# Kernel optimization log

Measured on AMD Instinct MI355X. Metric: run time of the kernel, lower is better.

Reference implementation:

```python
import jax, jax.numpy as jnp
import numpy as np

B, S, W = 16, 256, 128            # batch, seq_len (word pieces), words per sentence
V, H, L, NH, DH, FF, C = 30522, 768, 12, 12, 64, 3072, 425
EPS = 1e-12                        # HF Bert LayerNorm eps


def setup_inputs() -> dict:
    key = jax.random.key(0)
    kiter = iter(jax.random.split(key, 64))
    nk = lambda: next(kiter)
    # each word maps to 1 or 2 word-pieces -> total pieces in [W, 2W] <= S
    word_piece_tracked = jax.random.randint(nk(), (B, W), 1, 3)
    lengths = jnp.sum(word_piece_tracked, axis=1)
    encoded_batch = jax.random.randint(nk(), (B, S), 0, V)
    mask = (jnp.arange(S)[None, :] < lengths[:, None]).astype(jnp.int32)
    p = lambda *shape: jax.random.normal(nk(), shape, jnp.float32) * 0.02
    return dict(
        encoded_batch=encoded_batch, mask=mask, word_piece_tracked=word_piece_tracked,
        word_emb=p(V, H), pos_emb=p(S, H), type_emb=p(1, H),
        emb_ln_s=jnp.ones((H,), jnp.float32), emb_ln_b=jnp.zeros((H,), jnp.float32),
        Wq=p(L, H, H), bq=p(L, H), Wk=p(L, H, H), bk=p(L, H),
        Wv=p(L, H, H), bv=p(L, H), Wo=p(L, H, H), bo=p(L, H),
        ln1_s=jnp.ones((L, H), jnp.float32), ln1_b=jnp.zeros((L, H), jnp.float32),
        Wi=p(L, H, FF), bi=p(L, FF), Wo2=p(L, FF, H), bo2=p(L, H),
        ln2_s=jnp.ones((L, H), jnp.float32), ln2_b=jnp.zeros((L, H), jnp.float32),
        w1=p(H, 1024), b1=p(1024), w2=p(1024, C), b2=p(C),
    )


def _layer_norm(x, s, b):
    mu = jnp.mean(x, -1, keepdims=True)
    var = jnp.var(x, -1, keepdims=True)
    return (x - mu) * jax.lax.rsqrt(var + EPS) * s + b


def _forward(encoded_batch, mask, word_piece_tracked,
             word_emb, pos_emb, type_emb, emb_ln_s, emb_ln_b,
             Wq, bq, Wk, bk, Wv, bv, Wo, bo, ln1_s, ln1_b,
             Wi, bi, Wo2, bo2, ln2_s, ln2_b, w1, b1, w2, b2):
    # BERT embeddings (token_type all zeros)
    x = word_emb[encoded_batch] + pos_emb[None, :, :] + type_emb[0]
    x = _layer_norm(x, emb_ln_s, emb_ln_b)
    attn_bias = (1.0 - mask.astype(jnp.float32))[:, None, None, :] * -10000.0
    scale = 1.0 / np.sqrt(DH).astype(np.float32)

    def step(h, lp):
        wq, bq_, wk, bk_, wv, bv_, wo, bo_, l1s, l1b, wi, bi_, wo2, bo2_, l2s, l2b = lp
        q = (h @ wq + bq_).reshape(B, S, NH, DH)
        k = (h @ wk + bk_).reshape(B, S, NH, DH)
        v = (h @ wv + bv_).reshape(B, S, NH, DH)
        att = jax.nn.softmax(jnp.einsum('bqhd,bkhd->bhqk', q, k) * scale + attn_bias, axis=-1)
        ctx = jnp.einsum('bhqk,bkhd->bqhd', att, v).reshape(B, S, H)
        h = _layer_norm(h + ctx @ wo + bo_, l1s, l1b)
        ff = jax.nn.gelu(h @ wi + bi_, approximate=False)
        h = _layer_norm(h + ff @ wo2 + bo2_, l2s, l2b)
        return h, None

    x, _ = jax.lax.scan(step, x, (Wq, bq, Wk, bk, Wv, bv, Wo, bo, ln1_s, ln1_b,
                                  Wi, bi, Wo2, bo2, ln2_s, ln2_b))

    # MLP head (dropout = identity in eval)
    f1 = jax.nn.relu(x) @ w1 + b1          # [B, S, 1024]
    f2 = jax.nn.relu(f1) @ w2 + b2          # [B, S, C]

    # ragged segment-mean pooling over word pieces (equiv. to the python loop)
    cum = jnp.cumsum(word_piece_tracked, axis=1)                         # [B, W]
    seg = jax.vmap(lambda c: jnp.searchsorted(c, jnp.arange(S), side='right'))(cum)  # [B, S]
    sums = jax.vmap(lambda f, s: jax.ops.segment_sum(f, s, num_segments=W))(f2, seg)
    pooled = sums / word_piece_tracked[..., None].astype(f2.dtype)       # [B, W, C]
    out = jnp.concatenate([pooled, f2[:, W:, :]], axis=1)                # [B, S, C]
    return jax.nn.softmax(out, axis=2)


def reference(encoded_batch, mask, word_piece_tracked,
              word_emb, pos_emb, type_emb, emb_ln_s, emb_ln_b,
              Wq, bq, Wk, bk, Wv, bv, Wo, bo, ln1_s, ln1_b,
              Wi, bi, Wo2, bo2, ln2_s, ln2_b, w1, b1, w2, b2):
    return _forward(encoded_batch, mask, word_piece_tracked,
                    word_emb, pos_emb, type_emb, emb_ln_s, emb_ln_b,
                    Wq, bq, Wk, bk, Wv, bv, Wo, bo, ln1_s, ln1_b,
                    Wi, bi, Wo2, bo2, ln2_s, ln2_b, w1, b1, w2, b2)
```

## Files before the change

### kernel.cpp

```cpp
#include <hip/hip_runtime.h>
#include <math.h>

#define BB 16
#define SS 256
#define WW 128
#define HH 768
#define LL 12
#define NHH 12
#define DHH 64
#define FFD 3072
#define CC 425
#define NTOK (BB*SS)
#define QKVN (3*HH)

typedef __attribute__((ext_vector_type(8))) short bf16x8;
typedef __attribute__((ext_vector_type(4))) float f32x4;

__device__ __forceinline__ float bf2f(unsigned short u) {
    union { unsigned int i; float f; } z; z.i = ((unsigned int)u) << 16; return z.f;
}
__device__ __forceinline__ unsigned short f2bf(float f) {
    union { float f; unsigned int i; } z; z.f = f;
    unsigned int i = z.i;
    unsigned int r = (i + 0x7fffu + ((i >> 16) & 1u)) >> 16;
    return (unsigned short)r;
}

__device__ __forceinline__ void gload16(const void* g, void* l) {
    __builtin_amdgcn_global_load_lds((const __attribute__((address_space(1))) void*)g,
                                     (__attribute__((address_space(3))) void*)l, 16, 0, 0);
}

__device__ __forceinline__ float gelu_f(float v) {
    float ax = fabsf(v) * 0.70710678118654752f;
    float t = 1.0f / fmaf(0.3275911f, ax, 1.0f);
    float poly = t * fmaf(t, fmaf(t, fmaf(t, fmaf(t, 1.061405429f, -1.453152027f),
                                          1.421413741f), -0.284496736f), 0.254829592f);
    float er = 1.0f - poly * __expf(-ax * ax);
    er = (v < 0.f) ? -er : er;
    return 0.5f * v * (1.0f + er);
}

template<int BM, int BN, int ACT_C>
__launch_bounds__(256)
__global__ void gemm_bt(const unsigned short* __restrict__ A,
                        const unsigned short* __restrict__ Bt,
                        const float* __restrict__ bias,
                        unsigned short* __restrict__ Cm,
                        int M, int N, int K, int ldC) {
    constexpr bool BIG = (BM == 128 && BN == 128);
    constexpr int FM = BIG ? 4 : BM / 32;
    constexpr int FN = BIG ? 4 : BN / 32;
    constexpr int ASZ = BM * 32, BSZ = BN * 32;
    __shared__ __align__(16) unsigned short lA[2 * ASZ];
    __shared__ __align__(16) unsigned short lB[2 * BSZ];
    const int tid = threadIdx.x, w = tid >> 6, l = tid & 63;

    const int gx = gridDim.x;
    const int nwg = gx * gridDim.y;
    const int orig = blockIdx.y * gx + blockIdx.x;
    const int q = nwg >> 3, r = nwg & 7, xc = orig & 7, o8 = orig >> 3;
    const int wg = (xc < r ? xc * (q + 1) : r * (q + 1) + (xc - r) * q) + o8;
    const int m0 = (wg / gx) * BM, n0 = (wg % gx) * BN;

    const int wr = BIG ? (w >> 1) * 64 : (w >> 1) * (BM / 2);
    const int wc = BIG ? (w & 1) * 64 : (w & 1) * (BN / 2);
    const int lr = l & 15, lk = (l >> 4) * 8;
    const int rsw = ((lr >> 1) & 3) << 4;
    const int lrow = l >> 2;
    const int gs = (l & 3) ^ ((lrow >> 1) & 3);

    f32x4 acc[FM][FN];
#pragma unroll
    for (int m = 0; m < FM; ++m)
#pragma unroll
        for (int n = 0; n < FN; ++n) acc[m][n] = (f32x4){0.f, 0.f, 0.f, 0.f};

    auto stage = [&](int k0, unsigned short* dA, unsigned short* dB) {
#pragma unroll
        for (int it = 0; it < BM / 64; ++it) {
            int c = w * (BM / 64) + it;
            gload16(A + (size_t)(m0 + c * 16 + lrow) * K + k0 + gs * 8, dA + c * 512);
        }
#pragma unroll
        for (int it = 0; it < BN / 64; ++it) {
            int c = w * (BN / 64) + it;
            gload16(Bt + (size_t)(n0 + c * 16 + lrow) * K + k0 + gs * 8, dB + c * 512);
        }
    };

    const int nt = K >> 5;
    stage(0, lA, lB);
    __syncthreads();

    for (int t = 0; t < nt; ++t) {
        unsigned short* cA = lA + (t & 1) * ASZ;
        unsigned short* cB = lB + (t & 1) * BSZ;
        if (t + 1 < nt)
            stage((t + 1) << 5, lA + ((t + 1) & 1) * ASZ, lB + ((t + 1) & 1) * BSZ);
        bf16x8 af[FM], bfr[FN];
#pragma unroll
        for (int m = 0; m < FM; ++m) {
            int row = wr + m * 16 + lr;
            af[m] = *(const bf16x8*)((const char*)cA + row * 64 + ((lk * 2) ^ rsw));
        }
#pragma unroll
        for (int n = 0; n < FN; ++n) {
            int row = wc + n * 16 + lr;
            bfr[n] = *(const bf16x8*)((const char*)cB + row * 64 + ((lk * 2) ^ rsw));
        }
#pragma unroll
        for (int m = 0; m < FM; ++m)
#pragma unroll
            for (int n = 0; n < FN; ++n)
                acc[m][n] = __builtin_amdgcn_mfma_f32_16x16x32_bf16(af[m], bfr[n], acc[m][n], 0, 0, 0);
        __syncthreads();
    }

    const int orow = (l >> 4) * 4, ocol = l & 15;
#pragma unroll
    for (int m = 0; m < FM; ++m)
#pragma unroll
        for (int n = 0; n < FN; ++n) {
            int c = n0 + wc + n * 16 + ocol;
            if (c >= N) continue;
            float bb = bias[c];
#pragma unroll
            for (int j = 0; j < 4; ++j) {
                int rr = m0 + wr + m * 16 + orow + j;
                float vv = acc[m][n][j] + bb;
                if (ACT_C == 1) vv = gelu_f(vv);
                if (ACT_C == 2) vv = fmaxf(vv, 0.f);
                Cm[(size_t)rr * ldC + c] = f2bf(vv);
            }
        }
}

template<int ACT_A, int ACT_C>
__launch_bounds__(256)
__global__ void gemm_aw(const unsigned short* __restrict__ A,
                        const float* __restrict__ Wm,
                        const float* __restrict__ bias,
                        unsigned short* __restrict__ Cm,
                        int M, int N, int K, int ldC) {
    __shared__ __align__(16) unsigned short lA[64][40];
    __shared__ __align__(16) unsigned short lB[64][40];
    const int tid = threadIdx.x;
    const int m0 = blockIdx.y * 64;
    const int n0 = blockIdx.x * 64;
    const int w = tid >> 6, l = tid & 63;
    const int wr = (w >> 1) * 32, wc = (w & 1) * 32;
    const int lr = l & 15, lk = (l >> 4) * 8;

    f32x4 acc[2][2];
#pragma unroll
    for (int m = 0; m < 2; ++m)
#pragma unroll
        for (int n = 0; n < 2; ++n) acc[m][n] = (f32x4){0.f, 0.f, 0.f, 0.f};

    const int arow = tid >> 2, akc = (tid & 3) << 3;
    const int bkr = tid >> 3, bnc = (tid & 7) << 3;
    const bool nvec = (N & 7) == 0;

    for (int k0 = 0; k0 < K; k0 += 32) {
        uint4 av = *(const uint4*)(A + (size_t)(m0 + arow) * K + (k0 + akc));
        if (ACT_A) {
            unsigned short* p = (unsigned short*)&av;
#pragma unroll
            for (int j = 0; j < 8; ++j) if (p[j] & 0x8000u) p[j] = 0;
        }
        *(uint4*)&lA[arow][akc] = av;
        unsigned short bv[8];
        if (nvec) {
            const float* wp = Wm + (size_t)(k0 + bkr) * N + (n0 + bnc);
            float4 w0 = *(const float4*)(wp);
            float4 w1 = *(const float4*)(wp + 4);
            bv[0] = f2bf(w0.x); bv[1] = f2bf(w0.y); bv[2] = f2bf(w0.z); bv[3] = f2bf(w0.w);
            bv[4] = f2bf(w1.x); bv[5] = f2bf(w1.y); bv[6] = f2bf(w1.z); bv[7] = f2bf(w1.w);
        } else {
#pragma unroll
            for (int j = 0; j < 8; ++j) {
                int col = n0 + bnc + j;
                bv[j] = (col < N) ? f2bf(Wm[(size_t)(k0 + bkr) * N + col]) : (unsigned short)0;
            }
        }
#pragma unroll
        for (int j = 0; j < 8; ++j) lB[bnc + j][bkr] = bv[j];
        __syncthreads();

        bf16x8 af[2], bfr[2];
#pragma unroll
        for (int m = 0; m < 2; ++m) af[m] = *(const bf16x8*)&lA[wr + m * 16 + lr][lk];
#pragma unroll
        for (int n = 0; n < 2; ++n) bfr[n] = *(const bf16x8*)&lB[wc + n * 16 + lr][lk];
#pragma unroll
        for (int m = 0; m < 2; ++m)
#pragma unroll
            for (int n = 0; n < 2; ++n)
                acc[m][n] = __builtin_amdgcn_mfma_f32_16x16x32_bf16(af[m], bfr[n], acc[m][n], 0, 0, 0);
        __syncthreads();
    }

    const int orow = (l >> 4) * 4, ocol = l & 15;
#pragma unroll
    for (int m = 0; m < 2; ++m)
#pragma unroll
        for (int n = 0; n < 2; ++n) {
            int c = n0 + wc + n * 16 + ocol;
            if (c >= N) continue;
            float bb = bias[c];
#pragma unroll
            for (int j = 0; j < 4; ++j) {
                int r = m0 + wr + m * 16 + orow + j;
                float vv = acc[m][n][j] + bb;
                if (ACT_C == 1) vv = gelu_f(vv);
                if (ACT_C == 2) vv = fmaxf(vv, 0.f);
                Cm[(size_t)r * ldC + c] = f2bf(vv);
            }
        }
}

__global__ void transpose_w(const float* __restrict__ src, unsigned short* __restrict__ dst,
                            int K, int N, long srcLS, long dstLS) {
    int n0 = blockIdx.x * 32, k0 = blockIdx.y * 32;
    src += (size_t)blockIdx.z * srcLS;
    dst += (size_t)blockIdx.z * dstLS;
    __shared__ float tile[32][33];
    int tx = threadIdx.x & 31, ty = threadIdx.x >> 5;
#pragma unroll
    for (int r = 0; r < 4; ++r) {
        int k = k0 + ty + r * 8, n = n0 + tx;
        tile[ty + r * 8][tx] = (n < N && k < K) ? src[(size_t)k * N + n] : 0.f;
    }
    __syncthreads();
    int col2 = threadIdx.x & 15, rowb = threadIdx.x >> 4;
#pragma unroll
    for (int p = 0; p < 2; ++p) {
        int n = n0 + rowb + p * 16;
        unsigned int lo = f2bf(tile[col2 * 2][rowb + p * 16]);
        unsigned int hi = f2bf(tile[col2 * 2 + 1][rowb + p * 16]);
        *(unsigned int*)(dst + (size_t)n * K + k0 + col2 * 2) = lo | (hi << 16);
    }
}

__global__ void concat_bias(const float* bq, const float* bk, const float* bv, float* bqkv) {
    int i = blockIdx.x * 256 + threadIdx.x;
    if (i >= LL * QKVN) return;
    int lyr = i / QKVN, c = i % QKVN;
    float v = (c < HH) ? bq[lyr * HH + c] : (c < 2 * HH) ? bk[lyr * HH + c - HH] : bv[lyr * HH + c - 2 * HH];
    bqkv[i] = v;
}

__global__ void build_maskbias(const int* mask, float* mb) {
    int i = blockIdx.x * 256 + threadIdx.x;
    mb[i] = mask[i] ? 0.0f : -10000.0f;
}

__launch_bounds__(256)
__global__ void attention_mfma(const unsigned short* __restrict__ qkv,
                               const float* __restrict__ mb,
                               unsigned short* __restrict__ ctx) {
    const int qt = blockIdx.x, h = blockIdx.y, b = blockIdx.z;
    const int tid = threadIdx.x, w = tid >> 6, l = tid & 63;
    __shared__ __align__(16) unsigned short lK[SS * DHH];
    __shared__ __align__(16) unsigned short lVt[DHH * SS];
    const size_t tokbase = (size_t)b * SS * QKVN;

    {
        const unsigned short* kp = qkv + tokbase + (size_t)tid * QKVN + HH + h * DHH;
        const unsigned short* vp = kp + HH;
#pragma unroll
        for (int c = 0; c < 8; ++c) {
            uint4 kd = *(const uint4*)(kp + c * 8);
            *(uint4*)((char*)lK + ((tid * 128 + c * 16) ^ ((tid & 7) << 4))) = kd;
            uint4 vd = *(const uint4*)(vp + c * 8);
            const unsigned short* e = (const unsigned short*)&vd;
#pragma unroll
            for (int j = 0; j < 8; ++j) {
                int d = c * 8 + j;
                *(unsigned short*)((char*)lVt + ((d * 512 + tid * 2) ^ ((d & 7) << 4))) = e[j];
            }
        }
    }
    const int q0w = qt * 64 + w * 16;
    const unsigned short* qp = qkv + tokbase + (size_t)(q0w + (l & 15)) * QKVN + h * DHH + (l >> 4) * 8;
    bf16x8 aq0 = *(const bf16x8*)(qp);
    bf16x8 aq1 = *(const bf16x8*)(qp + 32);
    __syncthreads();

    f32x4 sc[16];
#pragma unroll
    for (int t = 0; t < 16; ++t) {
        int key = t * 16 + (l & 15);
        int base = key * 128;
        int sw = (key & 7) << 4;
        bf16x8 bk0 = *(const bf16x8*)((char*)lK + ((base + (l >> 4) * 16) ^ sw));
        bf16x8 bk1 = *(const bf16x8*)((char*)lK + ((base + 64 + (l >> 4) * 16) ^ sw));
        f32x4 a = (f32x4){0.f, 0.f, 0.f, 0.f};
        a = __builtin_amdgcn_mfma_f32_16x16x32_bf16(aq0, bk0, a, 0, 0, 0);
        a = __builtin_amdgcn_mfma_f32_16x16x32_bf16(aq1, bk1, a, 0, 0, 0);
        sc[t] = a;
    }
    const float* mbb = mb + b * SS;
    float mx[4] = {-3.0e38f, -3.0e38f, -3.0e38f, -3.0e38f};
#pragma unroll
    for (int t = 0; t < 16; ++t) {
        float mv = mbb[t * 16 + (l & 15)];
#pragma unroll
        for (int r = 0; r < 4; ++r) {
            float v = sc[t][r] * 0.125f + mv;
            sc[t][r] = v;
            mx[r] = fmaxf(mx[r], v);
        }
    }
#pragma unroll
    for (int m = 1; m <= 8; m <<= 1)
#pragma unroll
        for (int r = 0; r < 4; ++r) mx[r] = fmaxf(mx[r], __shfl_xor(mx[r], m));
    float sm[4] = {0.f, 0.f, 0.f, 0.f};
#pragma unroll
    for (int t = 0; t < 16; ++t)
#pragma unroll
        for (int r = 0; r < 4; ++r) {
            float e = __expf(sc[t][r] - mx[r]);
            sc[t][r] = e;
            sm[r] += e;
        }
#pragma unroll
    for (int m = 1; m <= 8; m <<= 1)
#pragma unroll
        for (int r = 0; r < 4; ++r) sm[r] += __shfl_xor(sm[r], m);
    float inv[4];
#pragma unroll
    for (int r = 0; r < 4; ++r) inv[r] = 1.0f / sm[r];

    __syncthreads();
    unsigned short* P = lK;
#pragma unroll
    for (int t = 0; t < 16; ++t)
#pragma unroll
        for (int r = 0; r < 4; ++r) {
            int prow = w * 16 + (l >> 4) * 4 + r;
            int pcol = t * 16 + (l & 15);
            *(unsigned short*)((char*)P + ((prow * 512 + pcol * 2) ^ ((prow & 7) << 4))) =
                f2bf(sc[t][r] * inv[r]);
        }
    __syncthreads();

    f32x4 o[4];
#pragma unroll
    for (int dt = 0; dt < 4; ++dt) o[dt] = (f32x4){0.f, 0.f, 0.f, 0.f};
#pragma unroll
    for (int kt = 0; kt < 8; ++kt) {
        int prow = w * 16 + (l & 15);
        int pkb = (kt * 32 + (l >> 4) * 8) * 2;
        bf16x8 pa = *(const bf16x8*)((char*)P + ((prow * 512 + pkb) ^ ((prow & 7) << 4)));
#pragma unroll
        for (int dt = 0; dt < 4; ++dt) {
            int d = dt * 16 + (l & 15);
            bf16x8 vb = *(const bf16x8*)((char*)lVt + ((d * 512 + pkb) ^ ((d & 7) << 4)));
            o[dt] = __builtin_amdgcn_mfma_f32_16x16x32_bf16(pa, vb, o[dt], 0, 0, 0);
        }
    }
#pragma unroll
    for (int dt = 0; dt < 4; ++dt)
#pragma unroll
        for (int r = 0; r < 4; ++r) {
            int q = qt * 64 + w * 16 + (l >> 4) * 4 + r;
            int d = dt * 16 + (l & 15);
            ctx[((size_t)(b * SS + q)) * HH + h * DHH + d] = f2bf(o[dt][r]);
        }
}

__global__ void embed_ln(const int* __restrict__ ids,
                         const float* __restrict__ we,
                         const float* __restrict__ pe,
                         const float* __restrict__ te,
                         const float* __restrict__ g,
                         const float* __restrict__ beta,
                         unsigned short* __restrict__ x) {
    int t = blockIdx.x, s = t % SS, tid = threadIdx.x;
    int id = ids[t];
    __shared__ float r1[256], r2[256];
    float e[3]; float sum = 0.f, sq = 0.f;
#pragma unroll
    for (int j = 0; j < 3; ++j) {
        int i = tid + j * 256;
        float v = we[(size_t)id * HH + i] + pe[(size_t)s * HH + i] + te[i];
        e[j] = v; sum += v; sq += v * v;
    }
    r1[tid] = sum; r2[tid] = sq; __syncthreads();
    for (int o = 128; o > 0; o >>= 1) {
        if (tid < o) { r1[tid] += r1[tid + o]; r2[tid] += r2[tid + o]; }
        __syncthreads();
    }
    float mu = r1[0] * (1.0f / HH);
    float var = fmaxf(r2[0] * (1.0f / HH) - mu * mu, 0.f);
    float rs = rsqrtf(var + 1e-12f);
#pragma unroll
    for (int j = 0; j < 3; ++j) {
        int i = tid + j * 256;
        x[(size_t)t * HH + i] = f2bf((e[j] - mu) * rs * g[i] + beta[i]);
    }
}

template<int WRITE_RELU>
__launch_bounds__(256)
__global__ void add_ln(unsigned short* __restrict__ x,
                       const unsigned short* __restrict__ y,
                       const float* __restrict__ g,
                       const float* __restrict__ beta,
                       unsigned short* __restrict__ xr) {
    const int t = blockIdx.x * 4 + (threadIdx.x >> 6);
    const int l = threadIdx.x & 63;
    const size_t base = (size_t)t * HH;
    float v[12];
    float sum = 0.f, sq = 0.f;
#pragma unroll
    for (int j = 0; j < 3; ++j) {
        uint2 xa = *(const uint2*)(x + base + j * 256 + l * 4);
        uint2 ya = *(const uint2*)(y + base + j * 256 + l * 4);
        const unsigned short* xp = (const unsigned short*)&xa;
        const unsigned short* yp = (const unsigned short*)&ya;
#pragma unroll
        for (int e = 0; e < 4; ++e) {
            float vv = bf2f(xp[e]) + bf2f(yp[e]);
            v[j * 4 + e] = vv;
            sum += vv; sq += vv * vv;
        }
    }
#pragma unroll
    for (int m = 1; m < 64; m <<= 1) {
        sum += __shfl_xor(sum, m);
        sq += __shfl_xor(sq, m);
    }
    float mu = sum * (1.0f / HH);
    float var = fmaxf(sq * (1.0f / HH) - mu * mu, 0.f);
    float rs = rsqrtf(var + 1e-12f);
#pragma unroll
    for (int j = 0; j < 3; ++j) {
        float4 gg = *(const float4*)(g + j * 256 + l * 4);
        float4 bb = *(const float4*)(beta + j * 256 + l * 4);
        float r0 = (v[j * 4 + 0] - mu) * rs * gg.x + bb.x;
        float r1 = (v[j * 4 + 1] - mu) * rs * gg.y + bb.y;
        float r2 = (v[j * 4 + 2] - mu) * rs * gg.z + bb.z;
        float r3 = (v[j * 4 + 3] - mu) * rs * gg.w + bb.w;
        uint2 st = {(unsigned)f2bf(r0) | ((unsigned)f2bf(r1) << 16),
                    (unsigned)f2bf(r2) | ((unsigned)f2bf(r3) << 16)};
        *(uint2*)(x + base + j * 256 + l * 4) = st;
        if (WRITE_RELU) {
            uint2 sr = {(unsigned)f2bf(fmaxf(r0, 0.f)) | ((unsigned)f2bf(fmaxf(r1, 0.f)) << 16),
                        (unsigned)f2bf(fmaxf(r2, 0.f)) | ((unsigned)f2bf(fmaxf(r3, 0.f)) << 16)};
            *(uint2*)(xr + base + j * 256 + l * 4) = sr;
        }
    }
}

__global__ void cumsum_k(const int* __restrict__ wpt, int* __restrict__ cum) {
    int b = blockIdx.x, w = threadIdx.x;
    int s = 0;
    for (int j = 0; j <= w; ++j) s += wpt[b * WW + j];
    cum[b * WW + w] = s;
}

__global__ void pool_softmax(const unsigned short* __restrict__ f2,
                             const int* __restrict__ cum,
                             float* __restrict__ out) {
    int t = blockIdx.x, b = t / SS, s = t % SS, tid = threadIdx.x;
    __shared__ float red[512];
    float val = -1e30f;
    bool act = tid < CC;
    if (act) {
        if (s < WW) {
            int end = cum[b * WW + s];
            int start = s ? cum[b * WW + s - 1] : 0;
            float su = 0.f;
            for (int j = start; j < end; ++j) su += bf2f(f2[((size_t)b * SS + j) * CC + tid]);
            val = su / (float)(end - start);
        } else {
            val = bf2f(f2[((size_t)b * SS + s) * CC + tid]);
        }
    }
    red[tid] = val; __syncthreads();
    for (int o = 256; o > 0; o >>= 1) {
        if (tid < o) red[tid] = fmaxf(red[tid], red[tid + o]);
        __syncthreads();
    }
    float mx = red[0]; __syncthreads();
    float e = act ? expf(val - mx) : 0.f;
    red[tid] = e; __syncthreads();
    for (int o = 256; o > 0; o >>= 1) {
        if (tid < o) red[tid] += red[tid + o];
        __syncthreads();
    }
    float inv = 1.0f / red[0];
    if (act) out[((size_t)b * SS + s) * CC + tid] = e * inv;
}

static inline size_t al256(size_t x) { return (x + 255) & ~(size_t)255; }

extern "C" void kernel_launch(void* const* d_in, const int* in_sizes, int n_in,
                              void* d_out, int out_size, void* d_ws, size_t ws_size,
                              hipStream_t stream) {
    const int* enc   = (const int*)d_in[0];
    const int* mask  = (const int*)d_in[1];
    const int* wpt   = (const int*)d_in[2];
    const float* word_emb = (const float*)d_in[3];
    const float* pos_emb  = (const float*)d_in[4];
    const float* type_emb = (const float*)d_in[5];
    const float* eln_s = (const float*)d_in[6];
    const float* eln_b = (const float*)d_in[7];
    const float* Wq = (const float*)d_in[8];
    const float* bq = (const float*)d_in[9];
    const float* Wk = (const float*)d_in[10];
    const float* bk = (const float*)d_in[11];
    const float* Wv = (const float*)d_in[12];
    const float* bv = (const float*)d_in[13];
    const float* Wo = (const float*)d_in[14];
    const float* bo = (const float*)d_in[15];
    const float* ln1s = (const float*)d_in[16];
    const float* ln1b = (const float*)d_in[17];
    const float* Wi = (const float*)d_in[18];
    const float* bi = (const float*)d_in[19];
    const float* Wo2 = (const float*)d_in[20];
    const float* bo2 = (const float*)d_in[21];
    const float* ln2s = (const float*)d_in[22];
    const float* ln2b = (const float*)d_in[23];
    const float* w1 = (const float*)d_in[24];
    const float* b1 = (const float*)d_in[25];
    const float* w2 = (const float*)d_in[26];
    const float* b2 = (const float*)d_in[27];

    unsigned char* ws = (unsigned char*)d_ws;
    size_t off = 0;
    unsigned short* x    = (unsigned short*)(ws + off); off = al256(off + (size_t)NTOK * HH * 2);
    unsigned short* qkv  = (unsigned short*)(ws + off); off = al256(off + (size_t)NTOK * QKVN * 2);
    unsigned short* ctx  = (unsigned short*)(ws + off); off = al256(off + (size_t)NTOK * HH * 2);
    unsigned short* proj = (unsigned short*)(ws + off); off = al256(off + (size_t)NTOK * HH * 2);
    unsigned short* ff   = (unsigned short*)(ws + off); off = al256(off + (size_t)NTOK * FFD * 2);
    unsigned short* f1   = (unsigned short*)(ws + off); off = al256(off + (size_t)NTOK * 1024 * 2);
    unsigned short* f2   = (unsigned short*)(ws + off); off = al256(off + (size_t)NTOK * CC * 2);
    unsigned short* xr   = (unsigned short*)(ws + off); off = al256(off + (size_t)NTOK * HH * 2);
    float* mb            = (float*)(ws + off);          off = al256(off + (size_t)NTOK * 4);
    int* cum             = (int*)(ws + off);            off = al256(off + (size_t)BB * WW * 4);
    float* bqkv          = (float*)(ws + off);          off = al256(off + (size_t)LL * QKVN * 4);
    size_t offFast = off;
    unsigned short* WqkvT = (unsigned short*)(ws + offFast); offFast = al256(offFast + (size_t)LL * QKVN * HH * 2);
    unsigned short* WoT   = (unsigned short*)(ws + offFast); offFast = al256(offFast + (size_t)LL * HH * HH * 2);
    unsigned short* WiT   = (unsigned short*)(ws + offFast); offFast = al256(offFast + (size_t)LL * FFD * HH * 2);
    unsigned short* Wo2T  = (unsigned short*)(ws + offFast); offFast = al256(offFast + (size_t)LL * HH * FFD * 2);
    unsigned short* w1T   = (unsigned short*)(ws + offFast); offFast = al256(offFast + (size_t)1024 * HH * 2);
    unsigned short* w2T   = (unsigned short*)(ws + offFast); offFast = al256(offFast + (size_t)512 * 1024 * 2);
    const bool fast = (ws_size >= offFast);

    build_maskbias<<<NTOK / 256, 256, 0, stream>>>(mask, mb);
    concat_bias<<<(LL * QKVN + 255) / 256, 256, 0, stream>>>(bq, bk, bv, bqkv);

    if (fast) {
        transpose_w<<<dim3(24, 24, LL), 256, 0, stream>>>(Wq, WqkvT, HH, HH, (long)HH * HH, (long)QKVN * HH);
        transpose_w<<<dim3(24, 24, LL), 256, 0, stream>>>(Wk, WqkvT + (size_t)HH * HH, HH, HH, (long)HH * HH, (long)QKVN * HH);
        transpose_w<<<dim3(24, 24, LL), 256, 0, stream>>>(Wv, WqkvT + (size_t)2 * HH * HH, HH, HH, (long)HH * HH, (long)QKVN * HH);
        transpose_w<<<dim3(24, 24, LL), 256, 0, stream>>>(Wo, WoT, HH, HH, (long)HH * HH, (long)HH * HH);
        transpose_w<<<dim3(96, 24, LL), 256, 0, stream>>>(Wi, WiT, HH, FFD, (long)HH * FFD, (long)FFD * HH);
        transpose_w<<<dim3(24, 96, LL), 256, 0, stream>>>(Wo2, Wo2T, FFD, HH, (long)FFD * HH, (long)HH * FFD);
        transpose_w<<<dim3(32, 24, 1), 256, 0, stream>>>(w1, w1T, HH, 1024, 0, 0);
        transpose_w<<<dim3(16, 32, 1), 256, 0, stream>>>(w2, w2T, 1024, CC, 0, 0);
    }

    embed_ln<<<NTOK, 256, 0, stream>>>(enc, word_emb, pos_emb, type_emb, eln_s, eln_b, x);

    const dim3 gQKV(QKVN / 128, NTOK / 128);
    const dim3 gWo(HH / 64, NTOK / 64);
    const dim3 gFF1(FFD / 128, NTOK / 128);
    const dim3 gFF2(HH / 64, NTOK / 64);
    const dim3 gH1(1024 / 64, NTOK / 64);
    const dim3 gH2(7, NTOK / 64);
    const dim3 gAttn(4, NHH, BB);

    for (int l = 0; l < LL; ++l) {
        if (fast) {
            gemm_bt<128, 128, 0><<<gQKV, 256, 0, stream>>>(x, WqkvT + (size_t)l * QKVN * HH, bqkv + l * QKVN, qkv, NTOK, QKVN, HH, QKVN);
        } else {
            const dim3 g64(HH / 64, NTOK / 64);
            gemm_aw<0, 0><<<g64, 256, 0, stream>>>(x, Wq + (size_t)l * HH * HH, bq + l * HH, qkv, NTOK, HH, HH, QKVN);
            gemm_aw<0, 0><<<g64, 256, 0, stream>>>(x, Wk + (size_t)l * HH * HH, bk + l * HH, qkv + HH, NTOK, HH, HH, QKVN);
            gemm_aw<0, 0><<<g64, 256, 0, stream>>>(x, Wv + (size_t)l * HH * HH, bv + l * HH, qkv + 2 * HH, NTOK, HH, HH, QKVN);
        }
        attention_mfma<<<gAttn, 256, 0, stream>>>(qkv, mb, ctx);
        if (fast) {
            gemm_bt<64, 64, 0><<<gWo, 256, 0, stream>>>(ctx, WoT + (size_t)l * HH * HH, bo + l * HH, proj, NTOK, HH, HH, HH);
        } else {
            gemm_aw<0, 0><<<dim3(HH / 64, NTOK / 64), 256, 0, stream>>>(ctx, Wo + (size_t)l * HH * HH, bo + l * HH, proj, NTOK, HH, HH, HH);
        }
        add_ln<0><<<NTOK / 4, 256, 0, stream>>>(x, proj, ln1s + l * HH, ln1b + l * HH, nullptr);
        if (fast) {
            gemm_bt<128, 128, 1><<<gFF1, 256, 0, stream>>>(x, WiT + (size_t)l * FFD * HH, bi + l * FFD, ff, NTOK, FFD, HH, FFD);
            gemm_bt<64, 64, 0><<<gFF2, 256, 0, stream>>>(ff, Wo2T + (size_t)l * HH * FFD, bo2 + l * HH, proj, NTOK, HH, FFD, HH);
        } else {
            gemm_aw<0, 1><<<dim3(FFD / 64, NTOK / 64), 256, 0, stream>>>(x, Wi + (size_t)l * HH * FFD, bi + l * FFD, ff, NTOK, FFD, HH, FFD);
            gemm_aw<0, 0><<<dim3(HH / 64, NTOK / 64), 256, 0, stream>>>(ff, Wo2 + (size_t)l * FFD * HH, bo2 + l * HH, proj, NTOK, HH, FFD, HH);
        }
        if (l == LL - 1)
            add_ln<1><<<NTOK / 4, 256, 0, stream>>>(x, proj, ln2s + l * HH, ln2b + l * HH, xr);
        else
            add_ln<0><<<NTOK / 4, 256, 0, stream>>>(x, proj, ln2s + l * HH, ln2b + l * HH, nullptr);
    }

    if (fast) {
        gemm_bt<64, 64, 2><<<gH1, 256, 0, stream>>>(xr, w1T, b1, f1, NTOK, 1024, HH, 1024);
        gemm_bt<64, 64, 0><<<gH2, 256, 0, stream>>>(f1, w2T, b2, f2, NTOK, CC, 1024, CC);
    } else {
        gemm_aw<0, 2><<<dim3(1024 / 64, NTOK / 64), 256, 0, stream>>>(xr, w1, b1, f1, NTOK, 1024, HH, 1024);
        gemm_aw<0, 0><<<dim3(7, NTOK / 64), 256, 0, stream>>>(f1, w2, b2, f2, NTOK, CC, 1024, CC);
    }
    cumsum_k<<<BB, WW, 0, stream>>>(wpt, cum);
    pool_softmax<<<NTOK, 512, 0, stream>>>(f2, cum, (float*)d_out);
}
```

Baseline: 2.159 ms.

## Split GEMM into 512-thread 128x128 and K64-staged 64x64 kernels

Replaces the templated gemm_bt with two specialised kernels. The 128x128 tile kernel now runs 8 waves per block (512 threads), each computing a 64x32 sub-tile, which raises wave-level parallelism and halves per-wave accumulator registers. The 64x64 kernel stages 64 K-elements per pipeline step instead of 32, halving the number of barriers and loop iterations per tile. The trade-off is more LDS per block for the 64x64 kernel and less per-wave operand reuse in the 128 kernel.

```diff
diff --git a/kernel.cpp b/kernel.cpp
--- a/kernel.cpp
+++ b/kernel.cpp
@@ -41,52 +41,42 @@
     return 0.5f * v * (1.0f + er);
 }
 
-template<int BM, int BN, int ACT_C>
-__launch_bounds__(256)
-__global__ void gemm_bt(const unsigned short* __restrict__ A,
+__device__ __forceinline__ int xcd_remap(int nwg, int orig) {
+    int q = nwg >> 3, r = nwg & 7, xc = orig & 7, o8 = orig >> 3;
+    return (xc < r ? xc * (q + 1) : r * (q + 1) + (xc - r) * q) + o8;
+}
+
+template<int ACT_C>
+__launch_bounds__(512)
+__global__ void gemm128(const unsigned short* __restrict__ A,
                         const unsigned short* __restrict__ Bt,
                         const float* __restrict__ bias,
                         unsigned short* __restrict__ Cm,
                         int M, int N, int K, int ldC) {
-    constexpr bool BIG = (BM == 128 && BN == 128);
-    constexpr int FM = BIG ? 4 : BM / 32;
-    constexpr int FN = BIG ? 4 : BN / 32;
-    constexpr int ASZ = BM * 32, BSZ = BN * 32;
-    __shared__ __align__(16) unsigned short lA[2 * ASZ];
-    __shared__ __align__(16) unsigned short lB[2 * BSZ];
+    constexpr int BUFS = 128 * 32;
+    __shared__ __align__(16) unsigned short lA[2 * BUFS];
+    __shared__ __align__(16) unsigned short lB[2 * BUFS];
     const int tid = threadIdx.x, w = tid >> 6, l = tid & 63;
 
     const int gx = gridDim.x;
-    const int nwg = gx * gridDim.y;
-    const int orig = blockIdx.y * gx + blockIdx.x;
-    const int q = nwg >> 3, r = nwg & 7, xc = orig & 7, o8 = orig >> 3;
-    const int wg = (xc < r ? xc * (q + 1) : r * (q + 1) + (xc - r) * q) + o8;
-    const int m0 = (wg / gx) * BM, n0 = (wg % gx) * BN;
-
-    const int wr = BIG ? (w >> 1) * 64 : (w >> 1) * (BM / 2);
-    const int wc = BIG ? (w & 1) * 64 : (w & 1) * (BN / 2);
+    const int wg = xcd_remap(gx * gridDim.y, blockIdx.y * gx + blockIdx.x);
+    const int m0 = (wg / gx) * 128, n0 = (wg % gx) * 128;
+
+    const int wr = (w >> 2) * 64, wc = (w & 3) * 32;
     const int lr = l & 15, lk = (l >> 4) * 8;
     const int rsw = ((lr >> 1) & 3) << 4;
     const int lrow = l >> 2;
     const int gs = (l & 3) ^ ((lrow >> 1) & 3);
 
-    f32x4 acc[FM][FN];
-#pragma unroll
-    for (int m = 0; m < FM; ++m)
-#pragma unroll
-        for (int n = 0; n < FN; ++n) acc[m][n] = (f32x4){0.f, 0.f, 0.f, 0.f};
+    f32x4 acc[4][2];
+#pragma unroll
+    for (int m = 0; m < 4; ++m)
+#pragma unroll
+        for (int n = 0; n < 2; ++n) acc[m][n] = (f32x4){0.f, 0.f, 0.f, 0.f};
 
     auto stage = [&](int k0, unsigned short* dA, unsigned short* dB) {
-#pragma unroll
-        for (int it = 0; it < BM / 64; ++it) {
-            int c = w * (BM / 64) + it;
-            gload16(A + (size_t)(m0 + c * 16 + lrow) * K + k0 + gs * 8, dA + c * 512);
-        }
-#pragma unroll
-        for (int it = 0; it < BN / 64; ++it) {
-            int c = w * (BN / 64) + it;
-            gload16(Bt + (size_t)(n0 + c * 16 + lrow) * K + k0 + gs * 8, dB + c * 512);
-        }
+        gload16(A + (size_t)(m0 + w * 16 + lrow) * K + k0 + gs * 8, dA + w * 512);
+        gload16(Bt + (size_t)(n0 + w * 16 + lrow) * K + k0 + gs * 8, dB + w * 512);
     };
 
     const int nt = K >> 5;
@@ -94,34 +84,122 @@
     __syncthreads();
 
     for (int t = 0; t < nt; ++t) {
-        unsigned short* cA = lA + (t & 1) * ASZ;
-        unsigned short* cB = lB + (t & 1) * BSZ;
+        unsigned short* cA = lA + (t & 1) * BUFS;
+        unsigned short* cB = lB + (t & 1) * BUFS;
         if (t + 1 < nt)
-            stage((t + 1) << 5, lA + ((t + 1) & 1) * ASZ, lB + ((t + 1) & 1) * BSZ);
-        bf16x8 af[FM], bfr[FN];
-#pragma unroll
-        for (int m = 0; m < FM; ++m) {
+            stage((t + 1) << 5, lA + ((t + 1) & 1) * BUFS, lB + ((t + 1) & 1) * BUFS);
+        bf16x8 af[4], bfr[2];
+#pragma unroll
+        for (int m = 0; m < 4; ++m) {
             int row = wr + m * 16 + lr;
             af[m] = *(const bf16x8*)((const char*)cA + row * 64 + ((lk * 2) ^ rsw));
         }
 #pragma unroll
-        for (int n = 0; n < FN; ++n) {
+        for (int n = 0; n < 2; ++n) {
             int row = wc + n * 16 + lr;
             bfr[n] = *(const bf16x8*)((const char*)cB + row * 64 + ((lk * 2) ^ rsw));
         }
 #pragma unroll
-        for (int m = 0; m < FM; ++m)
-#pragma unroll
-            for (int n = 0; n < FN; ++n)
+        for (int m = 0; m < 4; ++m)
+#pragma unroll
+            for (int n = 0; n < 2; ++n)
                 acc[m][n] = __builtin_amdgcn_mfma_f32_16x16x32_bf16(af[m], bfr[n], acc[m][n], 0, 0, 0);
         __syncthreads();
     }
 
     const int orow = (l >> 4) * 4, ocol = l & 15;
 #pragma unroll
-    for (int m = 0; m < FM; ++m)
-#pragma unroll
-        for (int n = 0; n < FN; ++n) {
+    for (int m = 0; m < 4; ++m)
+#pragma unroll
+        for (int n = 0; n < 2; ++n) {
+            int c = n0 + wc + n * 16 + ocol;
+            if (c >= N) continue;
+            float bb = bias[c];
+#pragma unroll
+            for (int j = 0; j < 4; ++j) {
+                int rr = m0 + wr + m * 16 + orow + j;
+                float vv = acc[m][n][j] + bb;
+                if (ACT_C == 1) vv = gelu_f(vv);
+                if (ACT_C == 2) vv = fmaxf(vv, 0.f);
+                Cm[(size_t)rr * ldC + c] = f2bf(vv);
+            }
+        }
+}
+
+template<int ACT_C>
+__launch_bounds__(256)
+__global__ void gemm64(const unsigned short* __restrict__ A,
+                       const unsigned short* __restrict__ Bt,
+                       const float* __restrict__ bias,
+                       unsigned short* __restrict__ Cm,
+                       int M, int N, int K, int ldC) {
+    constexpr int BUFS = 2 * 64 * 32;
+    __shared__ __align__(16) unsigned short lA[2 * BUFS];
+    __shared__ __align__(16) unsigned short lB[2 * BUFS];
+    const int tid = threadIdx.x, w = tid >> 6, l = tid & 63;
+
+    const int gx = gridDim.x;
+    const int wg = xcd_remap(gx * gridDim.y, blockIdx.y * gx + blockIdx.x);
+    const int m0 = (wg / gx) * 64, n0 = (wg % gx) * 64;
+
+    const int wr = (w >> 1) * 32, wc = (w & 1) * 32;
+    const int lr = l & 15, lk = (l >> 4) * 8;
+    const int rsw = ((lr >> 1) & 3) << 4;
+    const int lrow = l >> 2;
+    const int gs = (l & 3) ^ ((lrow >> 1) & 3);
+
+    f32x4 acc[2][2];
+#pragma unroll
+    for (int m = 0; m < 2; ++m)
+#pragma unroll
+        for (int n = 0; n < 2; ++n) acc[m][n] = (f32x4){0.f, 0.f, 0.f, 0.f};
+
+    auto stage = [&](int k0, unsigned short* dA, unsigned short* dB) {
+#pragma unroll
+        for (int h = 0; h < 2; ++h) {
+            gload16(A + (size_t)(m0 + w * 16 + lrow) * K + k0 + h * 32 + gs * 8,
+                    dA + h * 2048 + w * 512);
+            gload16(Bt + (size_t)(n0 + w * 16 + lrow) * K + k0 + h * 32 + gs * 8,
+                    dB + h * 2048 + w * 512);
+        }
+    };
+
+    const int nt = K >> 6;
+    stage(0, lA, lB);
+    __syncthreads();
+
+    for (int t = 0; t < nt; ++t) {
+        unsigned short* cA = lA + (t & 1) * BUFS;
+        unsigned short* cB = lB + (t & 1) * BUFS;
+        if (t + 1 < nt)
+            stage((t + 1) << 6, lA + ((t + 1) & 1) * BUFS, lB + ((t + 1) & 1) * BUFS);
+#pragma unroll
+        for (int h = 0; h < 2; ++h) {
+            bf16x8 af[2], bfr[2];
+#pragma unroll
+            for (int m = 0; m < 2; ++m) {
+                int row = wr + m * 16 + lr;
+                af[m] = *(const bf16x8*)((const char*)cA + h * 4096 + row * 64 + ((lk * 2) ^ rsw));
+            }
+#pragma unroll
+            for (int n = 0; n < 2; ++n) {
+                int row = wc + n * 16 + lr;
+                bfr[n] = *(const bf16x8*)((const char*)cB + h * 4096 + row * 64 + ((lk * 2) ^ rsw));
+            }
+#pragma unroll
+            for (int m = 0; m < 2; ++m)
+#pragma unroll
+                for (int n = 0; n < 2; ++n)
+                    acc[m][n] = __builtin_amdgcn_mfma_f32_16x16x32_bf16(af[m], bfr[n], acc[m][n], 0, 0, 0);
+        }
+        __syncthreads();
+    }
+
+    const int orow = (l >> 4) * 4, ocol = l & 15;
+#pragma unroll
+    for (int m = 0; m < 2; ++m)
+#pragma unroll
+        for (int n = 0; n < 2; ++n) {
             int c = n0 + wc + n * 16 + ocol;
             if (c >= N) continue;
             float bb = bias[c];
@@ -579,7 +657,7 @@
 
     for (int l = 0; l < LL; ++l) {
         if (fast) {
-            gemm_bt<128, 128, 0><<<gQKV, 256, 0, stream>>>(x, WqkvT + (size_t)l * QKVN * HH, bqkv + l * QKVN, qkv, NTOK, QKVN, HH, QKVN);
+            gemm128<0><<<gQKV, 512, 0, stream>>>(x, WqkvT + (size_t)l * QKVN * HH, bqkv + l * QKVN, qkv, NTOK, QKVN, HH, QKVN);
         } else {
             const dim3 g64(HH / 64, NTOK / 64);
             gemm_aw<0, 0><<<g64, 256, 0, stream>>>(x, Wq + (size_t)l * HH * HH, bq + l * HH, qkv, NTOK, HH, HH, QKVN);
@@ -588,14 +666,14 @@
         }
         attention_mfma<<<gAttn, 256, 0, stream>>>(qkv, mb, ctx);
         if (fast) {
-            gemm_bt<64, 64, 0><<<gWo, 256, 0, stream>>>(ctx, WoT + (size_t)l * HH * HH, bo + l * HH, proj, NTOK, HH, HH, HH);
+            gemm64<0><<<gWo, 256, 0, stream>>>(ctx, WoT + (size_t)l * HH * HH, bo + l * HH, proj, NTOK, HH, HH, HH);
         } else {
             gemm_aw<0, 0><<<dim3(HH / 64, NTOK / 64), 256, 0, stream>>>(ctx, Wo + (size_t)l * HH * HH, bo + l * HH, proj, NTOK, HH, HH, HH);
         }
         add_ln<0><<<NTOK / 4, 256, 0, stream>>>(x, proj, ln1s + l * HH, ln1b + l * HH, nullptr);
         if (fast) {
-            gemm_bt<128, 128, 1><<<gFF1, 256, 0, stream>>>(x, WiT + (size_t)l * FFD * HH, bi + l * FFD, ff, NTOK, FFD, HH, FFD);
-            gemm_bt<64, 64, 0><<<gFF2, 256, 0, stream>>>(ff, Wo2T + (size_t)l * HH * FFD, bo2 + l * HH, proj, NTOK, HH, FFD, HH);
+            gemm128<1><<<gFF1, 512, 0, stream>>>(x, WiT + (size_t)l * FFD * HH, bi + l * FFD, ff, NTOK, FFD, HH, FFD);
+            gemm64<0><<<gFF2, 256, 0, stream>>>(ff, Wo2T + (size_t)l * HH * FFD, bo2 + l * HH, proj, NTOK, HH, FFD, HH);
         } else {
             gemm_aw<0, 1><<<dim3(FFD / 64, NTOK / 64), 256, 0, stream>>>(x, Wi + (size_t)l * HH * FFD, bi + l * FFD, ff, NTOK, FFD, HH, FFD);
             gemm_aw<0, 0><<<dim3(HH / 64, NTOK / 64), 256, 0, stream>>>(ff, Wo2 + (size_t)l * FFD * HH, bo2 + l * HH, proj, NTOK, HH, FFD, HH);
@@ -607,8 +685,8 @@
     }
 
     if (fast) {
-        gemm_bt<64, 64, 2><<<gH1, 256, 0, stream>>>(xr, w1T, b1, f1, NTOK, 1024, HH, 1024);
-        gemm_bt<64, 64, 0><<<gH2, 256, 0, stream>>>(f1, w2T, b2, f2, NTOK, CC, 1024, CC);
+        gemm64<2><<<gH1, 256, 0, stream>>>(xr, w1T, b1, f1, NTOK, 1024, HH, 1024);
+        gemm64<0><<<gH2, 256, 0, stream>>>(f1, w2T, b2, f2, NTOK, CC, 1024, CC);
     } else {
         gemm_aw<0, 2><<<dim3(1024 / 64, NTOK / 64), 256, 0, stream>>>(xr, w1, b1, f1, NTOK, 1024, HH, 1024);
         gemm_aw<0, 0><<<dim3(7, NTOK / 64), 256, 0, stream>>>(f1, w2, b2, f2, NTOK, CC, 1024, CC);
```

New measurement: 1.997 ms (median of 2 runs). -7.5%, faster.
